# Performance work log

Measured on AMD Instinct MI355X. Metric: run time of the kernel, lower is better.

Reference implementation:

```python
import jax, jax.numpy as jnp
import numpy as np

D_MODEL = 96
N_HEAD = 3
HEAD_DIM = D_MODEL // N_HEAD  # 32
D_FF = 2048
WIDTH = 65
HALF_W = (WIDTH - 1) // 2  # 32
EPS = 1e-5


def layer_norm(x, g, b):
    mu = jnp.mean(x, axis=-1, keepdims=True)
    var = jnp.mean(jnp.square(x - mu), axis=-1, keepdims=True)
    return (x - mu) * jax.lax.rsqrt(var + EPS) * g + b


def setup_inputs() -> dict:
    key = jax.random.key(0)
    ks = jax.random.split(key, 8)
    B, T = 8, 2048
    s = 0.05
    return {
        "x": jax.random.normal(ks[0], (B, D_MODEL, T), dtype=jnp.float32),
        "w_qkv": jax.random.normal(ks[1], (3 * D_MODEL, D_MODEL), dtype=jnp.float32) * s,
        "b_qkv": jnp.zeros((3 * D_MODEL,), dtype=jnp.float32),
        "w_out": jax.random.normal(ks[2], (D_MODEL, D_MODEL), dtype=jnp.float32) * s,
        "b_out": jnp.zeros((D_MODEL,), dtype=jnp.float32),
        "ln1_g": jnp.ones((D_MODEL,), dtype=jnp.float32),
        "ln1_b": jnp.zeros((D_MODEL,), dtype=jnp.float32),
        "w_ff1": jax.random.normal(ks[3], (D_FF, D_MODEL), dtype=jnp.float32) * s,
        "b_ff1": jnp.zeros((D_FF,), dtype=jnp.float32),
        "w_ff2": jax.random.normal(ks[4], (D_MODEL, D_FF), dtype=jnp.float32) * s,
        "b_ff2": jnp.zeros((D_MODEL,), dtype=jnp.float32),
        "ln2_g": jnp.ones((D_MODEL,), dtype=jnp.float32),
        "ln2_b": jnp.zeros((D_MODEL,), dtype=jnp.float32),
        "lnf_g": jnp.ones((D_MODEL,), dtype=jnp.float32),
        "lnf_b": jnp.zeros((D_MODEL,), dtype=jnp.float32),
    }


def reference(x, w_qkv, b_qkv, w_out, b_out, ln1_g, ln1_b, w_ff1, b_ff1,
              w_ff2, b_ff2, ln2_g, ln2_b, lnf_g, lnf_b):
    # x: (B, C, T) -> (B, T, C)
    h = jnp.transpose(x, (0, 2, 1))
    B, T, C = h.shape

    # --- multi-head self-attention with banded mask ---
    qkv = h @ w_qkv.T + b_qkv                      # (B, T, 3C)
    q, k, v = jnp.split(qkv, 3, axis=-1)
    q = q.reshape(B, T, N_HEAD, HEAD_DIM)
    k = k.reshape(B, T, N_HEAD, HEAD_DIM)
    v = v.reshape(B, T, N_HEAD, HEAD_DIM)

    scale = 1.0 / jnp.sqrt(jnp.float32(HEAD_DIM))
    scores = jnp.einsum("bthd,bshd->bhts", q, k) * scale  # (B, H, T, T)

    idx = jnp.arange(T)
    band = jnp.abs(idx[:, None] - idx[None, :]) <= HALF_W  # |i-j| <= half width
    scores = jnp.where(band[None, None], scores, jnp.float32(-jnp.inf))

    attn = jax.nn.softmax(scores, axis=-1)
    ctx = jnp.einsum("bhts,bshd->bthd", attn, v).reshape(B, T, C)
    attn_out = ctx @ w_out.T + b_out

    # --- post-norm encoder layer (dropout inactive / eval mode) ---
    h = layer_norm(h + attn_out, ln1_g, ln1_b)
    ff = jax.nn.relu(h @ w_ff1.T + b_ff1) @ w_ff2.T + b_ff2
    h = layer_norm(h + ff, ln2_g, ln2_b)

    # extra layernorm applied when width is not None
    h = layer_norm(h, lnf_g, lnf_b)

    # (B, T, C) -> (B, C, T)
    return jnp.transpose(h, (0, 2, 1))
```

## Files before the change

kernel.cpp:

```cpp
#include <hip/hip_runtime.h>
#include <hip/hip_bf16.h>

#define B 8
#define T 2048
#define C 96
#define NH 3
#define HD 32
#define FFD 2048
#define HALF_W 32
#define BT (B*T)

typedef __hip_bfloat16 bf16;
typedef __attribute__((ext_vector_type(8))) short short8;
typedef __attribute__((ext_vector_type(4))) short short4v;
typedef __attribute__((ext_vector_type(16))) float floatx16;

__device__ __forceinline__ short f2bs(float v){
    __hip_bfloat16 h = __float2bfloat16(v);
    return *reinterpret_cast<short*>(&h);
}
__device__ __forceinline__ float bs2f(short s){
    unsigned u = ((unsigned)(unsigned short)s) << 16;
    return __uint_as_float(u);
}
__device__ __forceinline__ int imin(int a, int b){ return a < b ? a : b; }
__device__ __forceinline__ int imax(int a, int b){ return a > b ? a : b; }
__device__ __forceinline__ short8 ld_b64x2(const short* p){
    short4v a = *(const short4v*)p;
    short4v b = *(const short4v*)(p + 4);
    short8 v;
    v[0]=a[0]; v[1]=a[1]; v[2]=a[2]; v[3]=a[3];
    v[4]=b[0]; v[5]=b[1]; v[6]=b[2]; v[7]=b[3];
    return v;
}

__global__ void cvtw_kernel(const float* __restrict__ wq, const float* __restrict__ wo,
                            const float* __restrict__ w1, const float* __restrict__ w2,
                            bf16* __restrict__ dst){
    int i = blockIdx.x*256 + threadIdx.x;
    if(i < 27648){
        int e = i&7, lane = (i>>3)&63, r = i>>9;
        int ks = r%6, ot = r/6;
        int o = ot*32 + (lane&31);
        int k = ks*16 + (lane>>5)*8 + e;
        dst[i] = __float2bfloat16(wq[o*96 + k]);
    } else if(i < 36864){
        int j = i - 27648;
        int e = j&7, lane = (j>>3)&63, r = j>>9;
        int ks = r%6, ct = r/6;
        int c = ct*32 + (lane&31);
        int k = ks*16 + (lane>>5)*8 + e;
        dst[i] = __float2bfloat16(wo[c*96 + k]);
    } else if(i < 233472){
        int j = i - 36864;
        int e = j&7, lane = (j>>3)&63, r = j>>9;
        int ks = r%6; r /= 6;
        int w = r%4, jt = r/4;
        int row = jt*128 + w*32 + (lane&31);
        int k = ks*16 + (lane>>5)*8 + e;
        dst[i] = __float2bfloat16(w1[row*96 + k]);
    } else if(i < 430080){
        int j = i - 233472;
        int e = j&7, lane = (j>>3)&63, r = j>>9;
        int ct = r%3; r /= 3;
        int g = r%2; r /= 2;
        int w = r%4, jt = r/4;
        int c = ct*32 + (lane&31);
        int k = jt*128 + w*32 + g*16 + (lane>>5)*8 + e;
        dst[i] = __float2bfloat16(w2[c*FFD + k]);
    }
}

__global__ __launch_bounds__(256) void qkv_kernel(
    const float* __restrict__ x, const bf16* __restrict__ wqs,
    const float* __restrict__ bias, bf16* __restrict__ qswz,
    bf16* __restrict__ kswz, bf16* __restrict__ vbuf){
    __shared__ float xs[96*36];
    int b  = blockIdx.x >> 6;
    int tt = blockIdx.x & 63;
    int t0 = tt * 32;
    for(int e = threadIdx.x; e < 96*8; e += 256){
        int c = e >> 3, t4 = e & 7;
        *(float4*)(xs + c*36 + t4*4) =
            *(const float4*)(x + (size_t)b*C*T + (size_t)c*T + t0 + t4*4);
    }
    __syncthreads();
    const int w = threadIdx.x >> 6, lane = threadIdx.x & 63;
    const int lm = lane & 31, hq = lane >> 5;
    short8 bfr[6];
    #pragma unroll
    for(int ks = 0; ks < 6; ++ks){
        short8 v;
        #pragma unroll
        for(int i = 0; i < 8; ++i)
            v[i] = f2bs(xs[(ks*16 + hq*8 + i)*36 + lm]);
        bfr[ks] = v;
    }
    int nacc = (w == 0) ? 3 : 2;
    int ots[3] = {w, w+4, 8};
    floatx16 acc[3];
    #pragma unroll
    for(int i = 0; i < 3; ++i)
        #pragma unroll
        for(int r = 0; r < 16; ++r) acc[i][r] = 0.f;
    #pragma unroll
    for(int i = 0; i < 3; ++i){
        if(i < nacc){
            #pragma unroll
            for(int ks = 0; ks < 6; ++ks){
                short8 af = *(const short8*)((const short*)wqs
                              + (size_t)(ots[i]*6 + ks)*512 + lane*8);
                acc[i] = __builtin_amdgcn_mfma_f32_32x32x16_bf16(af, bfr[ks], acc[i], 0,0,0);
            }
        }
    }
    #pragma unroll
    for(int i = 0; i < 3; ++i){
        if(i < nacc){
            int ot = ots[i];
            int pkq[4][2];
            #pragma unroll
            for(int q = 0; q < 4; ++q){
                float4 bv = *(const float4*)(bias + ot*32 + 8*q + 4*hq);
                short4v t;
                t[0] = f2bs(acc[i][4*q+0] + bv.x);
                t[1] = f2bs(acc[i][4*q+1] + bv.y);
                t[2] = f2bs(acc[i][4*q+2] + bv.z);
                t[3] = f2bs(acc[i][4*q+3] + bv.w);
                int2 u = *(int2*)&t;
                pkq[q][0] = u.x; pkq[q][1] = u.y;
            }
            if(ot < 6){
                int type = ot/3, hh = ot%3;
                short* base = (short*)(type == 0 ? qswz : kswz)
                            + ((size_t)(b*NH + hh)*64 + tt)*1024 + lane*8;
                #pragma unroll
                for(int g = 0; g < 2; ++g){
                    int a0 = pkq[2*g][0],   a1 = pkq[2*g][1];
                    int b0 = pkq[2*g+1][0], b1v = pkq[2*g+1][1];
                    int ra0 = __shfl_xor(a0, 32),  ra1 = __shfl_xor(a1, 32);
                    int rb0 = __shfl_xor(b0, 32),  rb1 = __shfl_xor(b1v, 32);
                    int4 sfi;
                    sfi.x = hq ? rb0 : a0;
                    sfi.y = hq ? rb1 : a1;
                    sfi.z = hq ? b0  : ra0;
                    sfi.w = hq ? b1v : ra1;
                    *(int4*)(base + g*512) = sfi;
                }
            } else {
                int hh = ot - 6;
                short* rowp = (short*)vbuf + ((size_t)(b*NH + hh)*T + t0 + lm)*32;
                #pragma unroll
                for(int q = 0; q < 4; ++q){
                    int2 u; u.x = pkq[q][0]; u.y = pkq[q][1];
                    *(int2*)(rowp + 8*q + 4*hq) = u;
                }
            }
        }
    }
}

__global__ __launch_bounds__(192) void attn_op_kernel(
    const bf16* __restrict__ qswz, const bf16* __restrict__ kswz,
    const bf16* __restrict__ vbuf, const bf16* __restrict__ wos,
    const float* __restrict__ bias, const float* __restrict__ x,
    const float* __restrict__ g1, const float* __restrict__ bb1,
    bf16* __restrict__ h1b){
    __shared__ __align__(16) short VtS[3*3200];
    __shared__ __align__(16) short PtS[3][3200];
    __shared__ float LsS[3][32];
    __shared__ __align__(16) short ctxS[32*100];
    __shared__ float red1[2][3][32];
    const int tid = threadIdx.x;
    const int w = tid / 64, lane = tid & 63;
    const int lm = lane & 31, hq = lane >> 5;
    int b  = blockIdx.x >> 6;
    int tt = blockIdx.x & 63;
    int t0 = tt * 32;

    short8 wof[6];
    #pragma unroll
    for(int ks = 0; ks < 6; ++ks)
        wof[ks] = *(const short8*)((const short*)wos + (size_t)(w*6 + ks)*512 + lane*8);

    for(int e = tid; e < 576; e += 192){
        int hh = e / 192, rem = e % 192;
        int kp = rem >> 2, d8 = rem & 3;
        const short* vb = (const short*)vbuf + (size_t)(b*NH + hh)*T*32;
        int sa = imin(imax(t0 - 32 + 2*kp, 0), T-1);
        int sb = imin(imax(t0 - 32 + 2*kp + 1, 0), T-1);
        short8 va = *(const short8*)(vb + (size_t)sa*32 + d8*8);
        short8 v2 = *(const short8*)(vb + (size_t)sb*32 + d8*8);
        #pragma unroll
        for(int j = 0; j < 8; ++j){
            int val = (int)(unsigned short)va[j] | ((int)(unsigned short)v2[j] << 16);
            *(int*)(VtS + hh*3200 + (d8*8 + j)*100 + 2*kp) = val;
        }
    }
    const short* qsw = (const short*)qswz + ((size_t)(b*NH + w)*64 + tt)*1024 + lane*8;
    short8 qf0 = *(const short8*)(qsw);
    short8 qf1 = *(const short8*)(qsw + 512);
    floatx16 S[3];
    #pragma unroll
    for(int sub = 0; sub < 3; ++sub){
        int kt = imin(imax(tt - 1 + sub, 0), 63);
        const short* ksw = (const short*)kswz + ((size_t)(b*NH + w)*64 + kt)*1024 + lane*8;
        short8 kf0 = *(const short8*)(ksw);
        short8 kf1 = *(const short8*)(ksw + 512);
        floatx16 z;
        #pragma unroll
        for(int r = 0; r < 16; ++r) z[r] = 0.f;
        z = __builtin_amdgcn_mfma_f32_32x32x16_bf16(kf0, qf0, z, 0,0,0);
        z = __builtin_amdgcn_mfma_f32_32x32x16_bf16(kf1, qf1, z, 0,0,0);
        S[sub] = z;
    }
    const float scale = 0.17677669529663687f;
    float part = 0.f;
    #pragma unroll
    for(int sub = 0; sub < 3; ++sub){
        #pragma unroll
        for(int r = 0; r < 16; ++r){
            int key_local = sub*32 + (r&3) + 8*(r>>2) + 4*hq;
            int s_glob = t0 - 32 + key_local;
            int rel = key_local - lm;
            bool ok = (rel >= 0) && (rel <= 64) && (s_glob >= 0) && (s_glob < T);
            float p = ok ? __expf(S[sub][r]*scale) : 0.f;
            S[sub][r] = p;
            part += p;
        }
    }
    float ltot = part + __shfl_xor(part, 32);
    if(hq == 0) LsS[w][lm] = ltot;
    #pragma unroll
    for(int sub = 0; sub < 3; ++sub){
        #pragma unroll
        for(int q4 = 0; q4 < 4; ++q4){
            int kbase = sub*32 + 8*q4 + 4*hq;
            short4v pk;
            pk[0] = f2bs(S[sub][4*q4+0]);
            pk[1] = f2bs(S[sub][4*q4+1]);
            pk[2] = f2bs(S[sub][4*q4+2]);
            pk[3] = f2bs(S[sub][4*q4+3]);
            *(short4v*)(PtS[w] + lm*100 + kbase) = pk;
        }
    }
    __syncthreads();
    floatx16 O;
    #pragma unroll
    for(int r = 0; r < 16; ++r) O[r] = 0.f;
    #pragma unroll
    for(int ks = 0; ks < 6; ++ks){
        short8 pa = ld_b64x2(PtS[w] + lm*100 + ks*16 + hq*8);
        short8 vf = ld_b64x2(VtS + w*3200 + lm*100 + ks*16 + hq*8);
        O = __builtin_amdgcn_mfma_f32_32x32x16_bf16(pa, vf, O, 0,0,0);
    }
    #pragma unroll
    for(int r = 0; r < 16; ++r){
        int qr = (r&3) + 8*(r>>2) + 4*hq;
        float linv = 1.f / LsS[w][qr];
        ctxS[qr*100 + w*32 + lm] = f2bs(O[r]*linv);
    }
    __syncthreads();

    short8 bfr[6];
    #pragma unroll
    for(int ks = 0; ks < 6; ++ks)
        bfr[ks] = ld_b64x2(ctxS + lm*100 + ks*16 + hq*8);
    floatx16 acc;
    #pragma unroll
    for(int r = 0; r < 16; ++r) acc[r] = 0.f;
    #pragma unroll
    for(int ks = 0; ks < 6; ++ks)
        acc = __builtin_amdgcn_mfma_f32_32x32x16_bf16(wof[ks], bfr[ks], acc, 0,0,0);
    float vals[16];
    float p1 = 0.f, p2 = 0.f;
    #pragma unroll
    for(int q = 0; q < 4; ++q){
        int c = w*32 + 8*q + 4*hq;
        float4 bv = *(const float4*)(bias + c);
        float bva[4] = {bv.x, bv.y, bv.z, bv.w};
        #pragma unroll
        for(int r = 0; r < 4; ++r){
            float xv = x[(size_t)b*C*T + (size_t)(c + r)*T + t0 + lm];
            float v = acc[4*q+r] + bva[r] + xv;
            vals[4*q+r] = v;
            p1 += v; p2 += v*v;
        }
    }
    p1 += __shfl_xor(p1, 32);
    p2 += __shfl_xor(p2, 32);
    if(hq == 0){ red1[0][w][lm] = p1; red1[1][w][lm] = p2; }
    __syncthreads();
    float s  = red1[0][0][lm] + red1[0][1][lm] + red1[0][2][lm];
    float s2 = red1[1][0][lm] + red1[1][1][lm] + red1[1][2][lm];
    float mu = s * (1.0f/96.0f);
    float rstd = rsqrtf(s2*(1.0f/96.0f) - mu*mu + 1e-5f);
    int row = b*T + t0 + lm;
    #pragma unroll
    for(int q = 0; q < 4; ++q){
        int c = w*32 + 8*q + 4*hq;
        float4 gv = *(const float4*)(g1 + c);
        float4 bv = *(const float4*)(bb1 + c);
        float ga[4] = {gv.x, gv.y, gv.z, gv.w};
        float ba[4] = {bv.x, bv.y, bv.z, bv.w};
        short4v pk;
        #pragma unroll
        for(int r = 0; r < 4; ++r)
            pk[r] = f2bs((vals[4*q+r] - mu)*rstd*ga[r] + ba[r]);
        *(short4v*)((short*)h1b + (size_t)row*96 + c) = pk;
    }
}

__global__ __launch_bounds__(256, 1) void ff_ln_kernel(
    const bf16* __restrict__ h1b,
    const bf16* __restrict__ w1s, const float* __restrict__ b1,
    const bf16* __restrict__ w2s, const float* __restrict__ b2,
    const float* __restrict__ g2, const float* __restrict__ bt2,
    const float* __restrict__ gf, const float* __restrict__ btf,
    float* __restrict__ out){
    __shared__ float redp[4*2*3*1088];
    __shared__ float zt[96*65];
    const int tid = threadIdx.x;
    const int w4 = tid >> 6, lane = tid & 63;
    const int lm = lane & 31, hq = lane >> 5;
    const int r0 = blockIdx.x * 64;
    short8 hf[2][6];
    #pragma unroll
    for(int mt = 0; mt < 2; ++mt)
        #pragma unroll
        for(int ks = 0; ks < 6; ++ks)
            hf[mt][ks] = *(const short8*)((const short*)h1b
                       + (size_t)(r0 + mt*32 + lm)*96 + ks*16 + hq*8);
    floatx16 acc2[2][3];
    #pragma unroll
    for(int mt = 0; mt < 2; ++mt)
        #pragma unroll
        for(int i = 0; i < 3; ++i)
            #pragma unroll
            for(int r = 0; r < 16; ++r) acc2[mt][i][r] = 0.f;

    const short* w1p = (const short*)w1s + (size_t)w4*6*512 + lane*8;
    const short* w2p = (const short*)w2s + (size_t)w4*2*3*512 + lane*8;
    short8 cw1[6], cw2[6];
    #pragma unroll
    for(int ks = 0; ks < 6; ++ks)
        cw1[ks] = *(const short8*)(w1p + ks*512);
    #pragma unroll
    for(int g = 0; g < 2; ++g)
        #pragma unroll
        for(int ct = 0; ct < 3; ++ct)
            cw2[g*3 + ct] = *(const short8*)(w2p + ((size_t)g*3 + ct)*512);

    #pragma unroll
    for(int jt = 0; jt < 16; ++jt){
        const int jn = (jt + 1) & 15;
        short8 nw1[6], nw2[6];
        #pragma unroll
        for(int ks = 0; ks < 6; ++ks)
            nw1[ks] = *(const short8*)(w1p + (size_t)jn*4*6*512 + ks*512);
        #pragma unroll
        for(int g = 0; g < 2; ++g)
            #pragma unroll
            for(int ct = 0; ct < 3; ++ct)
                nw2[g*3 + ct] = *(const short8*)(w2p + ((size_t)jn*4*2*3 + g*3 + ct)*512);
        floatx16 a0, a1;
        #pragma unroll
        for(int r = 0; r < 16; ++r){ a0[r] = 0.f; a1[r] = 0.f; }
        #pragma unroll
        for(int ks = 0; ks < 6; ++ks){
            a0 = __builtin_amdgcn_mfma_f32_32x32x16_bf16(cw1[ks], hf[0][ks], a0, 0,0,0);
            a1 = __builtin_amdgcn_mfma_f32_32x32x16_bf16(cw1[ks], hf[1][ks], a1, 0,0,0);
        }
        int pk[2][4][2];
        #pragma unroll
        for(int q = 0; q < 4; ++q){
            float4 bv = *(const float4*)(b1 + jt*128 + w4*32 + 8*q + 4*hq);
            float bva[4] = {bv.x, bv.y, bv.z, bv.w};
            short4v t0v, t1v;
            #pragma unroll
            for(int r = 0; r < 4; ++r){
                float v0 = a0[4*q+r] + bva[r];
                float v1 = a1[4*q+r] + bva[r];
                t0v[r] = f2bs(v0 > 0.f ? v0 : 0.f);
                t1v[r] = f2bs(v1 > 0.f ? v1 : 0.f);
            }
            int2 u0 = *(int2*)&t0v; int2 u1 = *(int2*)&t1v;
            pk[0][q][0] = u0.x; pk[0][q][1] = u0.y;
            pk[1][q][0] = u1.x; pk[1][q][1] = u1.y;
        }
        #pragma unroll
        for(int g = 0; g < 2; ++g){
            short8 sf[2];
            #pragma unroll
            for(int mt = 0; mt < 2; ++mt){
                int a0i = pk[mt][2*g][0],   a1i = pk[mt][2*g][1];
                int b0i = pk[mt][2*g+1][0], b1i = pk[mt][2*g+1][1];
                int ra0 = __shfl_xor(a0i, 32), ra1 = __shfl_xor(a1i, 32);
                int rb0 = __shfl_xor(b0i, 32), rb1 = __shfl_xor(b1i, 32);
                int4 sfi;
                sfi.x = hq ? rb0 : a0i;
                sfi.y = hq ? rb1 : a1i;
                sfi.z = hq ? b0i : ra0;
                sfi.w = hq ? b1i : ra1;
                sf[mt] = *(short8*)&sfi;
            }
            #pragma unroll
            for(int ct = 0; ct < 3; ++ct){
                acc2[0][ct] = __builtin_amdgcn_mfma_f32_32x32x16_bf16(cw2[g*3+ct], sf[0], acc2[0][ct], 0,0,0);
                acc2[1][ct] = __builtin_amdgcn_mfma_f32_32x32x16_bf16(cw2[g*3+ct], sf[1], acc2[1][ct], 0,0,0);
            }
        }
        #pragma unroll
        for(int ks = 0; ks < 6; ++ks) cw1[ks] = nw1[ks];
        #pragma unroll
        for(int i = 0; i < 6; ++i) cw2[i] = nw2[i];
    }
    __syncthreads();
    #pragma unroll
    for(int mt = 0; mt < 2; ++mt)
        #pragma unroll
        for(int ct = 0; ct < 3; ++ct)
            #pragma unroll
            for(int q = 0; q < 4; ++q)
                #pragma unroll
                for(int r = 0; r < 4; ++r)
                    redp[((w4*2 + mt)*3 + ct)*1088 + lane*17 + 4*q + r] = acc2[mt][ct][4*q+r];
    __syncthreads();
    if(w4 < 2){
        const int mt = w4;
        const int rr = r0 + mt*32;
        float vals[48];
        float p1 = 0.f, p2 = 0.f;
        #pragma unroll
        for(int ct = 0; ct < 3; ++ct){
            #pragma unroll
            for(int q = 0; q < 4; ++q){
                int c = ct*32 + 8*q + 4*hq;
                float4 bv = *(const float4*)(b2 + c);
                short4v hv = *(const short4v*)((const short*)h1b + (size_t)(rr + lm)*96 + c);
                float bva[4] = {bv.x, bv.y, bv.z, bv.w};
                #pragma unroll
                for(int r = 0; r < 4; ++r){
                    float v = redp[((0*2 + mt)*3 + ct)*1088 + lane*17 + 4*q + r]
                            + redp[((1*2 + mt)*3 + ct)*1088 + lane*17 + 4*q + r]
                            + redp[((2*2 + mt)*3 + ct)*1088 + lane*17 + 4*q + r]
                            + redp[((3*2 + mt)*3 + ct)*1088 + lane*17 + 4*q + r]
                            + bva[r] + bs2f(hv[r]);
                    vals[ct*16 + 4*q + r] = v;
                    p1 += v; p2 += v*v;
                }
            }
        }
        p1 += __shfl_xor(p1, 32);
        p2 += __shfl_xor(p2, 32);
        float mu = p1*(1.0f/96.0f);
        float rstd = rsqrtf(p2*(1.0f/96.0f) - mu*mu + 1e-5f);
        float q1 = 0.f, q2 = 0.f;
        #pragma unroll
        for(int ct = 0; ct < 3; ++ct){
            #pragma unroll
            for(int q = 0; q < 4; ++q){
                int c = ct*32 + 8*q + 4*hq;
                float4 gv = *(const float4*)(g2 + c);
                float4 bv = *(const float4*)(bt2 + c);
                float ga[4] = {gv.x, gv.y, gv.z, gv.w};
                float ba[4] = {bv.x, bv.y, bv.z, bv.w};
                #pragma unroll
                for(int r = 0; r < 4; ++r){
                    float y = (vals[ct*16+4*q+r] - mu)*rstd*ga[r] + ba[r];
                    vals[ct*16+4*q+r] = y;
                    q1 += y; q2 += y*y;
                }
            }
        }
        q1 += __shfl_xor(q1, 32);
        q2 += __shfl_xor(q2, 32);
        float mu2 = q1*(1.0f/96.0f);
        float rstd2 = rsqrtf(q2*(1.0f/96.0f) - mu2*mu2 + 1e-5f);
        #pragma unroll
        for(int ct = 0; ct < 3; ++ct){
            #pragma unroll
            for(int q = 0; q < 4; ++q){
                int c = ct*32 + 8*q + 4*hq;
                float4 gv = *(const float4*)(gf + c);
                float4 bv = *(const float4*)(btf + c);
                float ga[4] = {gv.x, gv.y, gv.z, gv.w};
                float ba[4] = {bv.x, bv.y, bv.z, bv.w};
                #pragma unroll
                for(int r = 0; r < 4; ++r)
                    zt[(c + r)*65 + mt*32 + lm] = (vals[ct*16+4*q+r] - mu2)*rstd2*ga[r] + ba[r];
            }
        }
    }
    __syncthreads();
    int bb  = r0 / T;
    int t0g = r0 % T;
    for(int e = tid; e < 96*64; e += 256){
        int c = e >> 6, tt = e & 63;
        out[(size_t)bb*C*T + (size_t)c*T + t0g + tt] = zt[c*65 + tt];
    }
}

extern "C" void kernel_launch(void* const* d_in, const int* in_sizes, int n_in,
                              void* d_out, int out_size, void* d_ws, size_t ws_size,
                              hipStream_t stream) {
    const float* x     = (const float*)d_in[0];
    const float* w_qkv = (const float*)d_in[1];
    const float* b_qkv = (const float*)d_in[2];
    const float* w_out = (const float*)d_in[3];
    const float* b_out = (const float*)d_in[4];
    const float* ln1_g = (const float*)d_in[5];
    const float* ln1_b = (const float*)d_in[6];
    const float* w_ff1 = (const float*)d_in[7];
    const float* b_ff1 = (const float*)d_in[8];
    const float* w_ff2 = (const float*)d_in[9];
    const float* b_ff2 = (const float*)d_in[10];
    const float* ln2_g = (const float*)d_in[11];
    const float* ln2_b = (const float*)d_in[12];
    const float* lnf_g = (const float*)d_in[13];
    const float* lnf_b = (const float*)d_in[14];
    float* out = (float*)d_out;

    char* wsb = (char*)d_ws;
    bf16*  qswz  = (bf16*)wsb;
    bf16*  kswz  = (bf16*)(wsb + 3145728);
    bf16*  vbuf  = (bf16*)(wsb + 6291456);
    bf16*  h1b   = (bf16*)(wsb + 9437184);
    bf16*  wts   = (bf16*)(wsb + 12582912);
    bf16*  wqs   = wts;
    bf16*  wos   = wts + 27648;
    bf16*  w1s   = wts + 36864;
    bf16*  w2s   = wts + 233472;

    cvtw_kernel   <<<1680, 256, 0, stream>>>(w_qkv, w_out, w_ff1, w_ff2, wts);
    qkv_kernel    <<<BT/32, 256, 0, stream>>>(x, wqs, b_qkv, qswz, kswz, vbuf);
    attn_op_kernel<<<B*(T/32), 192, 0, stream>>>(qswz, kswz, vbuf, wos, b_out, x,
                                                 ln1_g, ln1_b, h1b);
    ff_ln_kernel  <<<BT/64, 256, 0, stream>>>(h1b, w1s, b_ff1, w2s, b_ff2,
                                              ln2_g, ln2_b, lnf_g, lnf_b, out);
}
```

Before: 126.6 us.

## Halve FF kernel row tile to 32, raise occupancy, spread LayerNorm across warps

The feed-forward kernel now processes 32 rows per block instead of 64, which doubles the grid to 512 blocks and allows two blocks per CU through launch_bounds(256,2). Halving the per-thread accumulators frees registers, and shared memory is reused between the reduction buffer and the output transpose tile. The LayerNorm epilogue is split across three warps with cross-warp reductions in shared memory, where before two warps each did full rows. The output store now writes float4. In exchange, the FF1/FF2 weights are streamed twice as often per row, and the epilogue needs extra barriers.

```diff
diff --git a/kernel.cpp b/kernel.cpp
--- a/kernel.cpp
+++ b/kernel.cpp
@@ -32,6 +32,16 @@
     v[0]=a[0]; v[1]=a[1]; v[2]=a[2]; v[3]=a[3];
     v[4]=b[0]; v[5]=b[1]; v[6]=b[2]; v[7]=b[3];
     return v;
+}
+__device__ __forceinline__ int4 exch_pair(int a0,int a1,int b0,int b1,int hq){
+    int ra0=__shfl_xor(a0,32), ra1=__shfl_xor(a1,32);
+    int rb0=__shfl_xor(b0,32), rb1=__shfl_xor(b1,32);
+    int4 s;
+    s.x = hq ? rb0 : a0;
+    s.y = hq ? rb1 : a1;
+    s.z = hq ? b0  : ra0;
+    s.w = hq ? b1  : ra1;
+    return s;
 }
 
 __global__ void cvtw_kernel(const float* __restrict__ wq, const float* __restrict__ wo,
@@ -311,193 +321,175 @@
     }
 }
 
-__global__ __launch_bounds__(256, 1) void ff_ln_kernel(
+__global__ __launch_bounds__(256, 2) void ff_kernel(
     const bf16* __restrict__ h1b,
     const bf16* __restrict__ w1s, const float* __restrict__ b1,
     const bf16* __restrict__ w2s, const float* __restrict__ b2,
     const float* __restrict__ g2, const float* __restrict__ bt2,
     const float* __restrict__ gf, const float* __restrict__ btf,
     float* __restrict__ out){
-    __shared__ float redp[4*2*3*1088];
-    __shared__ float zt[96*65];
+    __shared__ __align__(16) char smem[53760];
+    float* REDP = (float*)smem;
+    float* ZT   = (float*)smem;
+    float* RED1 = (float*)(smem + 52224);
+    float* RED2 = (float*)(smem + 52992);
+
     const int tid = threadIdx.x;
     const int w4 = tid >> 6, lane = tid & 63;
     const int lm = lane & 31, hq = lane >> 5;
-    const int r0 = blockIdx.x * 64;
-    short8 hf[2][6];
-    #pragma unroll
-    for(int mt = 0; mt < 2; ++mt)
+    const int r0 = blockIdx.x * 32;
+    const short* h1p = (const short*)h1b;
+
+    short8 hf[6];
+    #pragma unroll
+    for(int ks = 0; ks < 6; ++ks)
+        hf[ks] = *(const short8*)(h1p + (size_t)(r0 + lm)*96 + ks*16 + hq*8);
+
+    floatx16 acc2[3];
+    #pragma unroll
+    for(int i = 0; i < 3; ++i)
+        #pragma unroll
+        for(int r = 0; r < 16; ++r) acc2[i][r] = 0.f;
+
+    const short* w1b = (const short*)w1s + lane*8;
+    const short* w2b = (const short*)w2s + lane*8;
+    short8 cw1[6], cw2[6];
+    #pragma unroll
+    for(int ks = 0; ks < 6; ++ks)
+        cw1[ks] = *(const short8*)(w1b + (size_t)(w4*6 + ks)*512);
+    #pragma unroll
+    for(int g = 0; g < 2; ++g)
+        #pragma unroll
+        for(int ct = 0; ct < 3; ++ct)
+            cw2[g*3 + ct] = *(const short8*)(w2b + (size_t)((w4*2 + g)*3 + ct)*512);
+
+    #pragma unroll
+    for(int it = 0; it < 16; ++it){
+        const int J  = w4 + it*4;
+        const int Jn = (it < 15) ? J + 4 : w4;
+        short8 nw1[6], nw2[6];
         #pragma unroll
         for(int ks = 0; ks < 6; ++ks)
-            hf[mt][ks] = *(const short8*)((const short*)h1b
-                       + (size_t)(r0 + mt*32 + lm)*96 + ks*16 + hq*8);
-    floatx16 acc2[2][3];
-    #pragma unroll
-    for(int mt = 0; mt < 2; ++mt)
-        #pragma unroll
-        for(int i = 0; i < 3; ++i)
-            #pragma unroll
-            for(int r = 0; r < 16; ++r) acc2[mt][i][r] = 0.f;
-
-    const short* w1p = (const short*)w1s + (size_t)w4*6*512 + lane*8;
-    const short* w2p = (const short*)w2s + (size_t)w4*2*3*512 + lane*8;
-    short8 cw1[6], cw2[6];
-    #pragma unroll
-    for(int ks = 0; ks < 6; ++ks)
-        cw1[ks] = *(const short8*)(w1p + ks*512);
-    #pragma unroll
-    for(int g = 0; g < 2; ++g)
-        #pragma unroll
-        for(int ct = 0; ct < 3; ++ct)
-            cw2[g*3 + ct] = *(const short8*)(w2p + ((size_t)g*3 + ct)*512);
-
-    #pragma unroll
-    for(int jt = 0; jt < 16; ++jt){
-        const int jn = (jt + 1) & 15;
-        short8 nw1[6], nw2[6];
+            nw1[ks] = *(const short8*)(w1b + (size_t)(Jn*6 + ks)*512);
+        #pragma unroll
+        for(int g = 0; g < 2; ++g)
+            #pragma unroll
+            for(int ct = 0; ct < 3; ++ct)
+                nw2[g*3 + ct] = *(const short8*)(w2b + (size_t)((Jn*2 + g)*3 + ct)*512);
+        floatx16 a0;
+        #pragma unroll
+        for(int r = 0; r < 16; ++r) a0[r] = 0.f;
         #pragma unroll
         for(int ks = 0; ks < 6; ++ks)
-            nw1[ks] = *(const short8*)(w1p + (size_t)jn*4*6*512 + ks*512);
-        #pragma unroll
-        for(int g = 0; g < 2; ++g)
-            #pragma unroll
-            for(int ct = 0; ct < 3; ++ct)
-                nw2[g*3 + ct] = *(const short8*)(w2p + ((size_t)jn*4*2*3 + g*3 + ct)*512);
-        floatx16 a0, a1;
-        #pragma unroll
-        for(int r = 0; r < 16; ++r){ a0[r] = 0.f; a1[r] = 0.f; }
-        #pragma unroll
-        for(int ks = 0; ks < 6; ++ks){
-            a0 = __builtin_amdgcn_mfma_f32_32x32x16_bf16(cw1[ks], hf[0][ks], a0, 0,0,0);
-            a1 = __builtin_amdgcn_mfma_f32_32x32x16_bf16(cw1[ks], hf[1][ks], a1, 0,0,0);
-        }
-        int pk[2][4][2];
+            a0 = __builtin_amdgcn_mfma_f32_32x32x16_bf16(cw1[ks], hf[ks], a0, 0,0,0);
+        int pk[4][2];
         #pragma unroll
         for(int q = 0; q < 4; ++q){
-            float4 bv = *(const float4*)(b1 + jt*128 + w4*32 + 8*q + 4*hq);
+            float4 bv = *(const float4*)(b1 + J*32 + 8*q + 4*hq);
             float bva[4] = {bv.x, bv.y, bv.z, bv.w};
-            short4v t0v, t1v;
+            short4v tv;
             #pragma unroll
             for(int r = 0; r < 4; ++r){
                 float v0 = a0[4*q+r] + bva[r];
-                float v1 = a1[4*q+r] + bva[r];
-                t0v[r] = f2bs(v0 > 0.f ? v0 : 0.f);
-                t1v[r] = f2bs(v1 > 0.f ? v1 : 0.f);
+                tv[r] = f2bs(v0 > 0.f ? v0 : 0.f);
             }
-            int2 u0 = *(int2*)&t0v; int2 u1 = *(int2*)&t1v;
-            pk[0][q][0] = u0.x; pk[0][q][1] = u0.y;
-            pk[1][q][0] = u1.x; pk[1][q][1] = u1.y;
+            int2 uu = *(int2*)&tv; pk[q][0] = uu.x; pk[q][1] = uu.y;
         }
         #pragma unroll
         for(int g = 0; g < 2; ++g){
-            short8 sf[2];
-            #pragma unroll
-            for(int mt = 0; mt < 2; ++mt){
-                int a0i = pk[mt][2*g][0],   a1i = pk[mt][2*g][1];
-                int b0i = pk[mt][2*g+1][0], b1i = pk[mt][2*g+1][1];
-                int ra0 = __shfl_xor(a0i, 32), ra1 = __shfl_xor(a1i, 32);
-                int rb0 = __shfl_xor(b0i, 32), rb1 = __shfl_xor(b1i, 32);
-                int4 sfi;
-                sfi.x = hq ? rb0 : a0i;
-                sfi.y = hq ? rb1 : a1i;
-                sfi.z = hq ? b0i : ra0;
-                sfi.w = hq ? b1i : ra1;
-                sf[mt] = *(short8*)&sfi;
+            int4 sfi = exch_pair(pk[2*g][0], pk[2*g][1], pk[2*g+1][0], pk[2*g+1][1], hq);
+            short8 sf = *(short8*)&sfi;
+            #pragma unroll
+            for(int ct = 0; ct < 3; ++ct)
+                acc2[ct] = __builtin_amdgcn_mfma_f32_32x32x16_bf16(cw2[g*3+ct], sf, acc2[ct], 0,0,0);
+        }
+        #pragma unroll
+        for(int ks = 0; ks < 6; ++ks) cw1[ks] = nw1[ks];
+        #pragma unroll
+        for(int i = 0; i < 6; ++i) cw2[i] = nw2[i];
+    }
+    #pragma unroll
+    for(int ct = 0; ct < 3; ++ct)
+        #pragma unroll
+        for(int q = 0; q < 4; ++q)
+            #pragma unroll
+            for(int r = 0; r < 4; ++r)
+                REDP[(w4*3 + ct)*1088 + lane*17 + 4*q + r] = acc2[ct][4*q+r];
+    __syncthreads();
+
+    float fv[16];
+    float e1 = 0.f, e2 = 0.f;
+    if(w4 < 3){
+        #pragma unroll
+        for(int q = 0; q < 4; ++q){
+            int cb = w4*32 + 8*q + 4*hq;
+            float4 bv = *(const float4*)(b2 + cb);
+            float bva[4] = {bv.x, bv.y, bv.z, bv.w};
+            short4v hv = *(const short4v*)(h1p + (size_t)(r0 + lm)*96 + cb);
+            #pragma unroll
+            for(int r = 0; r < 4; ++r){
+                float v = REDP[(0*3 + w4)*1088 + lane*17 + 4*q + r]
+                        + REDP[(1*3 + w4)*1088 + lane*17 + 4*q + r]
+                        + REDP[(2*3 + w4)*1088 + lane*17 + 4*q + r]
+                        + REDP[(3*3 + w4)*1088 + lane*17 + 4*q + r]
+                        + bva[r] + bs2f(hv[r]);
+                fv[4*q+r] = v;
+                e1 += v; e2 += v*v;
             }
-            #pragma unroll
-            for(int ct = 0; ct < 3; ++ct){
-                acc2[0][ct] = __builtin_amdgcn_mfma_f32_32x32x16_bf16(cw2[g*3+ct], sf[0], acc2[0][ct], 0,0,0);
-                acc2[1][ct] = __builtin_amdgcn_mfma_f32_32x32x16_bf16(cw2[g*3+ct], sf[1], acc2[1][ct], 0,0,0);
+        }
+        e1 += __shfl_xor(e1, 32);
+        e2 += __shfl_xor(e2, 32);
+        if(hq == 0){ RED1[w4*32 + lm] = e1; RED1[96 + w4*32 + lm] = e2; }
+    }
+    __syncthreads();
+    float f1 = 0.f, f2 = 0.f;
+    if(w4 < 3){
+        float s  = RED1[lm] + RED1[32 + lm] + RED1[64 + lm];
+        float s2 = RED1[96 + lm] + RED1[128 + lm] + RED1[160 + lm];
+        float mu = s * (1.0f/96.0f);
+        float rstd = rsqrtf(s2*(1.0f/96.0f) - mu*mu + 1e-5f);
+        #pragma unroll
+        for(int q = 0; q < 4; ++q){
+            int c = w4*32 + 8*q + 4*hq;
+            float4 gv = *(const float4*)(g2 + c);
+            float4 bv = *(const float4*)(bt2 + c);
+            float ga[4] = {gv.x, gv.y, gv.z, gv.w};
+            float ba[4] = {bv.x, bv.y, bv.z, bv.w};
+            #pragma unroll
+            for(int r = 0; r < 4; ++r){
+                float y = (fv[4*q+r] - mu)*rstd*ga[r] + ba[r];
+                fv[4*q+r] = y;
+                f1 += y; f2 += y*y;
             }
         }
-        #pragma unroll
-        for(int ks = 0; ks < 6; ++ks) cw1[ks] = nw1[ks];
-        #pragma unroll
-        for(int i = 0; i < 6; ++i) cw2[i] = nw2[i];
-    }
-    __syncthreads();
-    #pragma unroll
-    for(int mt = 0; mt < 2; ++mt)
-        #pragma unroll
-        for(int ct = 0; ct < 3; ++ct)
-            #pragma unroll
-            for(int q = 0; q < 4; ++q)
-                #pragma unroll
-                for(int r = 0; r < 4; ++r)
-                    redp[((w4*2 + mt)*3 + ct)*1088 + lane*17 + 4*q + r] = acc2[mt][ct][4*q+r];
-    __syncthreads();
-    if(w4 < 2){
-        const int mt = w4;
-        const int rr = r0 + mt*32;
-        float vals[48];
-        float p1 = 0.f, p2 = 0.f;
-        #pragma unroll
-        for(int ct = 0; ct < 3; ++ct){
-            #pragma unroll
-            for(int q = 0; q < 4; ++q){
-                int c = ct*32 + 8*q + 4*hq;
-                float4 bv = *(const float4*)(b2 + c);
-                short4v hv = *(const short4v*)((const short*)h1b + (size_t)(rr + lm)*96 + c);
-                float bva[4] = {bv.x, bv.y, bv.z, bv.w};
-                #pragma unroll
-                for(int r = 0; r < 4; ++r){
-                    float v = redp[((0*2 + mt)*3 + ct)*1088 + lane*17 + 4*q + r]
-                            + redp[((1*2 + mt)*3 + ct)*1088 + lane*17 + 4*q + r]
-                            + redp[((2*2 + mt)*3 + ct)*1088 + lane*17 + 4*q + r]
-                            + redp[((3*2 + mt)*3 + ct)*1088 + lane*17 + 4*q + r]
-                            + bva[r] + bs2f(hv[r]);
-                    vals[ct*16 + 4*q + r] = v;
-                    p1 += v; p2 += v*v;
-                }
-            }
-        }
-        p1 += __shfl_xor(p1, 32);
-        p2 += __shfl_xor(p2, 32);
-        float mu = p1*(1.0f/96.0f);
-        float rstd = rsqrtf(p2*(1.0f/96.0f) - mu*mu + 1e-5f);
-        float q1 = 0.f, q2 = 0.f;
-        #pragma unroll
-        for(int ct = 0; ct < 3; ++ct){
-            #pragma unroll
-            for(int q = 0; q < 4; ++q){
-                int c = ct*32 + 8*q + 4*hq;
-                float4 gv = *(const float4*)(g2 + c);
-                float4 bv = *(const float4*)(bt2 + c);
-                float ga[4] = {gv.x, gv.y, gv.z, gv.w};
-                float ba[4] = {bv.x, bv.y, bv.z, bv.w};
-                #pragma unroll
-                for(int r = 0; r < 4; ++r){
-                    float y = (vals[ct*16+4*q+r] - mu)*rstd*ga[r] + ba[r];
-                    vals[ct*16+4*q+r] = y;
-                    q1 += y; q2 += y*y;
-                }
-            }
-        }
-        q1 += __shfl_xor(q1, 32);
-        q2 += __shfl_xor(q2, 32);
-        float mu2 = q1*(1.0f/96.0f);
-        float rstd2 = rsqrtf(q2*(1.0f/96.0f) - mu2*mu2 + 1e-5f);
-        #pragma unroll
-        for(int ct = 0; ct < 3; ++ct){
-            #pragma unroll
-            for(int q = 0; q < 4; ++q){
-                int c = ct*32 + 8*q + 4*hq;
-                float4 gv = *(const float4*)(gf + c);
-                float4 bv = *(const float4*)(btf + c);
-                float ga[4] = {gv.x, gv.y, gv.z, gv.w};
-                float ba[4] = {bv.x, bv.y, bv.z, bv.w};
-                #pragma unroll
-                for(int r = 0; r < 4; ++r)
-                    zt[(c + r)*65 + mt*32 + lm] = (vals[ct*16+4*q+r] - mu2)*rstd2*ga[r] + ba[r];
-            }
-        }
-    }
-    __syncthreads();
-    int bb  = r0 / T;
-    int t0g = r0 % T;
-    for(int e = tid; e < 96*64; e += 256){
-        int c = e >> 6, tt = e & 63;
-        out[(size_t)bb*C*T + (size_t)c*T + t0g + tt] = zt[c*65 + tt];
+        f1 += __shfl_xor(f1, 32);
+        f2 += __shfl_xor(f2, 32);
+        if(hq == 0){ RED2[w4*32 + lm] = f1; RED2[96 + w4*32 + lm] = f2; }
+    }
+    __syncthreads();
+    if(w4 < 3){
+        float s  = RED2[lm] + RED2[32 + lm] + RED2[64 + lm];
+        float s2 = RED2[96 + lm] + RED2[128 + lm] + RED2[160 + lm];
+        float mu = s * (1.0f/96.0f);
+        float rstd = rsqrtf(s2*(1.0f/96.0f) - mu*mu + 1e-5f);
+        #pragma unroll
+        for(int q = 0; q < 4; ++q){
+            int c = w4*32 + 8*q + 4*hq;
+            float4 gv = *(const float4*)(gf + c);
+            float4 bv = *(const float4*)(btf + c);
+            float ga[4] = {gv.x, gv.y, gv.z, gv.w};
+            float ba[4] = {bv.x, bv.y, bv.z, bv.w};
+            #pragma unroll
+            for(int r = 0; r < 4; ++r)
+                ZT[(c + r)*36 + lm] = (fv[4*q+r] - mu)*rstd*ga[r] + ba[r];
+        }
+    }
+    __syncthreads();
+    const int bb = r0 / T, t0g = r0 % T;
+    float* ob = out + (size_t)bb*C*T + t0g;
+    for(int e = tid; e < 96*8; e += 256){
+        int c = e >> 3, qq = e & 7;
+        *(float4*)(ob + (size_t)c*T + qq*4) = *(const float4*)(ZT + c*36 + qq*4);
     }
 }
 
@@ -536,6 +528,6 @@
     qkv_kernel    <<<BT/32, 256, 0, stream>>>(x, wqs, b_qkv, qswz, kswz, vbuf);
     attn_op_kernel<<<B*(T/32), 192, 0, stream>>>(qswz, kswz, vbuf, wos, b_out, x,
                                                  ln1_g, ln1_b, h1b);
-    ff_ln_kernel  <<<BT/64, 256, 0, stream>>>(h1b, w1s, b_ff1, w2s, b_ff2,
+    ff_kernel     <<<BT/32, 256, 0, stream>>>(h1b, w1s, b_ff1, w2s, b_ff2,
                                               ln2_g, ln2_b, lnf_g, lnf_b, out);
 }
```

Result: no change. 126.5 us (-0.0%).
